# Optimization experiments

Hardware: AMD Instinct MI355X
Metric: run time of the kernel (lower is better)

## Reference

```python
import jax, jax.numpy as jnp
import numpy as np

B, L, C = 2, 2048, 1024
DK, H = 64, 16

def setup_inputs() -> dict:
    key = jax.random.key(0)
    ks = jax.random.split(key, 12)
    def lin(kw, kb, out_dim, in_dim):
        w = jax.random.normal(kw, (out_dim, in_dim), jnp.float32) * (1.0 / np.sqrt(in_dim))
        b = jnp.zeros((out_dim,), jnp.float32)
        return w, b
    WQ_w, WQ_b = lin(ks[0], ks[1], DK * H, C)
    WK_w, WK_b = lin(ks[2], ks[3], DK * H, C)
    WV_w, WV_b = lin(ks[4], ks[5], DK * H, C)
    WO_w, WO_b = lin(ks[6], ks[7], C, DK * H)
    qx = jax.random.normal(ks[8], (B, L, C), jnp.float32)
    kx = jax.random.normal(ks[9], (B, L, C), jnp.float32)
    vx = jax.random.normal(ks[10], (B, L, C), jnp.float32)
    maskPAD = jax.random.randint(ks[11], (B, L, L), 0, 2, jnp.int32)
    return {"qx": qx, "kx": kx, "vx": vx, "maskPAD": maskPAD,
            "WQ_w": WQ_w, "WQ_b": WQ_b, "WK_w": WK_w, "WK_b": WK_b,
            "WV_w": WV_w, "WV_b": WV_b, "WO_w": WO_w, "WO_b": WO_b}

def reference(qx, kx, vx, maskPAD, WQ_w, WQ_b, WK_w, WK_b, WV_w, WV_b, WO_w, WO_b):
    Bq, qL, _ = qx.shape
    kvL = kx.shape[1]
    # projections -> [B, H, L, DK]
    q = (qx @ WQ_w.T + WQ_b).reshape(Bq, qL, H, DK).transpose(0, 2, 1, 3)
    k = (kx @ WK_w.T + WK_b).reshape(Bq, kvL, H, DK).transpose(0, 2, 1, 3)
    v = (vx @ WV_w.T + WV_b).reshape(Bq, kvL, H, DK).transpose(0, 2, 1, 3)
    scores = jnp.einsum('bhqd,bhkd->bhqk', q, k) / np.sqrt(DK).astype(np.float32)
    scores = jnp.where((maskPAD == 0)[:, None, :, :], jnp.float32(-2**15 + 1), scores)
    alpha = jax.nn.softmax(scores, axis=3)  # dropout p=0 (eval)
    z = jnp.einsum('bhqk,bhkd->bhqd', alpha, v)
    z = z.transpose(0, 2, 1, 3).reshape(Bq, qL, H * DK)
    return z @ WO_w.T + WO_b
```

## Files before the change

### kernel.cpp

```cpp
#include <hip/hip_runtime.h>
#include <stdint.h>
#include <math.h>

typedef short short8 __attribute__((ext_vector_type(8)));
typedef short short4v __attribute__((ext_vector_type(4)));
typedef float float4v __attribute__((ext_vector_type(4)));
typedef float float2v __attribute__((ext_vector_type(2)));

static __device__ __forceinline__ float bf2f(uint16_t u) {
    union { uint32_t i; float f; } x; x.i = ((uint32_t)u) << 16; return x.f;
}
static __device__ __forceinline__ uint16_t f2bf(float f) {
    union { float f; uint32_t i; } x; x.f = f;
    uint32_t u = x.i;
    u += 0x7FFFu + ((u >> 16) & 1u);
    return (uint16_t)(u >> 16);
}
static __device__ __forceinline__ uint16_t f2bf_sane(float f) {
    uint16_t u = f2bf(f);
    if ((u & 0x7F80u) == 0x7F80u) u = 0;
    return u;
}
static __device__ __forceinline__ float san_f32(float f) {
    union { float f; uint32_t i; } x; x.f = f;
    if (((x.i >> 23) & 0xFFu) == 0xFFu) return 0.f;
    return x.f;
}
static __device__ __forceinline__ void gll16(const void* g, void* l) {
    __builtin_amdgcn_global_load_lds((const __attribute__((address_space(1))) void*)g,
                                     (__attribute__((address_space(3))) void*)l,
                                     16, 0, 0);
}
static __device__ __forceinline__ short8 load8(const void* p, size_t off, int fp32) {
    if (!fp32) return *(const short8*)((const uint16_t*)p + off);
    const float* f = (const float*)p + off;
    const float4v a = *(const float4v*)f;
    const float4v b = *(const float4v*)(f + 4);
    short8 r;
    r[0] = (short)f2bf(a[0]); r[1] = (short)f2bf(a[1]);
    r[2] = (short)f2bf(a[2]); r[3] = (short)f2bf(a[3]);
    r[4] = (short)f2bf(b[0]); r[5] = (short)f2bf(b[1]);
    r[6] = (short)f2bf(b[2]); r[7] = (short)f2bf(b[3]);
    return r;
}

static __device__ __forceinline__ float fexp2(float x) {
#if __has_builtin(__builtin_amdgcn_exp2f)
    return __builtin_amdgcn_exp2f(x);
#else
    float r; asm("v_exp_f32 %0, %1\ns_nop 0" : "=v"(r) : "v"(x)); return r;
#endif
}

static __device__ __forceinline__ float maskexp2(float s, uint32_t nib, int r) {
    union { float f; uint32_t u; } x; x.f = s;
    const uint32_t keep = (uint32_t)(((int32_t)(nib << (31 - r))) >> 31);
    x.u = (x.u & keep) | (~keep & 0xFF800000u);
    return fexp2(x.f);
}

static __device__ __forceinline__ float4v mfma16_bf16(short4v a, short4v b, float4v c) {
#if __has_builtin(__builtin_amdgcn_mfma_f32_16x16x16bf16_1k)
    return __builtin_amdgcn_mfma_f32_16x16x16bf16_1k(a, b, c, 0, 0, 0);
#else
    float4v d = c;
    asm volatile("v_mfma_f32_16x16x16_bf16 %0, %1, %2, %0"
                 : "+v"(d) : "v"(a), "v"(b));
    return d;
#endif
}

__global__ __launch_bounds__(256) void pack_kernel(
    const int* __restrict__ mask, uint64_t* __restrict__ mask64,
    const uint16_t* __restrict__ qx, int* __restrict__ flag)
{
    const int wave = threadIdx.x >> 6, lane = threadIdx.x & 63;
    if (blockIdx.x == 1024) {
        __shared__ int s;
        const int tid = threadIdx.x;
        if (tid == 0) s = 0;
        __syncthreads();
        int bad = 0;
#pragma unroll 8
        for (int i = 0; i < 64; ++i) {
            const uint16_t u = qx[tid * 64 + i];
            bad |= ((u & 0x7F80u) == 0x7F80u) ? 1 : 0;
        }
        if (bad) atomicOr(&s, 1);
        __syncthreads();
        if (tid == 0) *flag = s;
        return;
    }
    const int row = blockIdx.x * 4 + wave;
    const int* src = mask + (size_t)row * 2048;
#pragma unroll 4
    for (int j = 0; j < 32; ++j) {
        const int m = src[j * 64 + lane];
        const uint64_t bal = __ballot(m != 0);
        if (lane == 0) mask64[(size_t)row * 32 + j] = bal;
    }
}

__global__ __launch_bounds__(256) void convert_kernel(
    const void* qx, const void* kx, const void* vx,
    const void* wq, const void* wk, const void* wv, const void* wo,
    const void* bq, const void* bk, const void* bv, const void* bo,
    uint16_t* cIn, uint16_t* cW, uint16_t* cB, const int* flag)
{
    const int mode = *flag;
    if (!mode) return;
    const int z = blockIdx.z;
    if (z < 3) {
        const void* src = (z == 0) ? qx : (z == 1) ? kx : vx;
        uint16_t* dst = cIn + (size_t)z * 4194304;
#pragma unroll
        for (int it = 0; it < 8; ++it) {
            const int idx8 = (blockIdx.x * 8 + it) * 256 + threadIdx.x;
            *(short8*)(dst + (size_t)idx8 * 8) = load8(src, (size_t)idx8 * 8, 1);
        }
    } else if (z < 7) {
        const int t = z - 3;
        const void* src = (t == 0) ? wq : (t == 1) ? wk : (t == 2) ? wv : wo;
        uint16_t* dst = cW + (size_t)t * 1048576;
#pragma unroll
        for (int it = 0; it < 2; ++it) {
            const int idx8 = (blockIdx.x * 2 + it) * 256 + threadIdx.x;
            *(short8*)(dst + (size_t)idx8 * 8) = load8(src, (size_t)idx8 * 8, 1);
        }
    } else {
        const int idx8 = blockIdx.x * 256 + threadIdx.x;
        if (idx8 < 128) {
#pragma unroll
            for (int t = 0; t < 4; ++t) {
                const void* src = (t == 0) ? bq : (t == 1) ? bk : (t == 2) ? bv : bo;
                *(short8*)(cB + t * 1024 + idx8 * 8) = load8(src, (size_t)idx8 * 8, 1);
            }
        }
    }
}

template <int MI, int NI>
static __device__ __forceinline__ void gemm_tile(
    const uint16_t* __restrict__ A, const uint16_t* __restrict__ W,
    const uint16_t* __restrict__ bias, void* __restrict__ C,
    int c_fp32, float out_scale)
{
    constexpr int TM = MI * 32, TN = NI * 32;
    __shared__ __align__(16) uint16_t sA[TM * 32];
    __shared__ __align__(16) uint16_t sB[TN * 32];

    const int tid  = threadIdx.x;
    const int wave = tid >> 6;
    const int lane = tid & 63;
    const int quad = lane >> 4;
    const int l15  = lane & 15;
    const int m0 = blockIdx.y * TM;
    const int n0 = blockIdx.x * TN;
    const int wm = (wave >> 1) * (MI * 16);
    const int wn = (wave & 1) * (NI * 16);
    const int r16 = lane >> 2;
    const int ch  = lane & 3;

    float4v acc[MI][NI] = {};

    for (int k0 = 0; k0 < 1024; k0 += 32) {
        __syncthreads();
#pragma unroll
        for (int g = wave; g < TM / 16; g += 4)
            gll16(A + (size_t)(m0 + g * 16 + r16) * 1024 + k0 + ch * 8,
                  (char*)sA + (size_t)g * 1024);
#pragma unroll
        for (int g = wave; g < TN / 16; g += 4)
            gll16(W + (size_t)(n0 + g * 16 + r16) * 1024 + k0 + ch * 8,
                  (char*)sB + (size_t)g * 1024);
        asm volatile("s_waitcnt vmcnt(0)" ::: "memory");
        __syncthreads();

        short8 af[MI], bfr[NI];
#pragma unroll
        for (int i = 0; i < MI; ++i)
            af[i] = *(const short8*)&sA[(wm + i * 16 + l15) * 32 + quad * 8];
#pragma unroll
        for (int j = 0; j < NI; ++j)
            bfr[j] = *(const short8*)&sB[(wn + j * 16 + l15) * 32 + quad * 8];
#pragma unroll
        for (int mi = 0; mi < MI; ++mi)
#pragma unroll
            for (int ni = 0; ni < NI; ++ni)
                acc[mi][ni] = __builtin_amdgcn_mfma_f32_16x16x32_bf16(
                    af[mi], bfr[ni], acc[mi][ni], 0, 0, 0);
    }

#pragma unroll
    for (int ni = 0; ni < NI; ++ni) {
        const int n = n0 + wn + ni * 16 + l15;
        const float bv = bf2f(bias[n]);
#pragma unroll
        for (int mi = 0; mi < MI; ++mi) {
            const int mbase = m0 + wm + mi * 16 + quad * 4;
#pragma unroll
            for (int r = 0; r < 4; ++r) {
                const float v = (acc[mi][ni][r] + bv) * out_scale;
                const size_t idx = (size_t)(mbase + r) * 1024 + n;
                if (c_fp32) ((float*)C)[idx] = san_f32(v);
                else        ((uint16_t*)C)[idx] = f2bf_sane(v);
            }
        }
    }
}

__global__ __launch_bounds__(256) void qkv_kernel(
    const uint16_t* rqx, const uint16_t* rkx, const uint16_t* rvx,
    const uint16_t* rwq, const uint16_t* rwk, const uint16_t* rwv,
    const uint16_t* rbq, const uint16_t* rbk, const uint16_t* rbv,
    const uint16_t* cIn, const uint16_t* cW, const uint16_t* cB,
    uint16_t* Q, uint16_t* K, uint16_t* V, const int* flag)
{
    const int mode = *flag;
    const int z = blockIdx.z;
    const uint16_t* A = mode ? cIn + (size_t)z * 4194304
                             : ((z == 0) ? rqx : (z == 1) ? rkx : rvx);
    const uint16_t* W = mode ? cW + (size_t)z * 1048576
                             : ((z == 0) ? rwq : (z == 1) ? rwk : rwv);
    const uint16_t* b = mode ? cB + z * 1024
                             : ((z == 0) ? rbq : (z == 1) ? rbk : rbv);
    uint16_t* C = (z == 0) ? Q : (z == 1) ? K : V;
    const float sc = (z == 0) ? 0.18033688f : 1.0f;
    gemm_tile<4, 4>(A, W, b, C, 0, sc);
}

__global__ __launch_bounds__(256) void out_kernel(
    const uint16_t* Z, const uint16_t* rwo, const uint16_t* rbo,
    const uint16_t* cW, const uint16_t* cB, void* out, const int* flag)
{
    const int mode = *flag;
    const uint16_t* W = mode ? cW + 3 * 1048576 : rwo;
    const uint16_t* b = mode ? cB + 3 * 1024 : rbo;
    gemm_tile<2, 4>(Z, W, b, out, mode, 1.0f);
}

__global__ __launch_bounds__(256) void vtrans_kernel(
    const uint16_t* __restrict__ Vp, uint16_t* __restrict__ Vt)
{
    __shared__ __align__(16) uint16_t t[64][72];
    const int tid = threadIdx.x;
    const int lt = blockIdx.x, h = blockIdx.y, b = blockIdx.z;
#pragma unroll
    for (int p = 0; p < 2; ++p) {
        const int r = p * 32 + (tid >> 3);
        const int c = (tid & 7) * 8;
        *(short8*)&t[r][c] =
            *(const short8*)(Vp + (size_t)(b * 2048 + lt * 64 + r) * 1024 + h * 64 + c);
    }
    __syncthreads();
#pragma unroll
    for (int p = 0; p < 2; ++p) {
        const int d = p * 32 + (tid >> 3);
        const int c = (tid & 7) * 8;
        short8 v;
#pragma unroll
        for (int j = 0; j < 8; ++j) v[j] = (short)t[c + j][d];
        *(short8*)(Vt + (size_t)((b * 16 + h) * 64 + d) * 2048 + lt * 64 + c) = v;
    }
}

#define VS 72

__global__ __launch_bounds__(256, 4) void attn_kernel(
    const uint16_t* __restrict__ Q, const uint16_t* __restrict__ Kp,
    const uint16_t* __restrict__ Vt, const uint64_t* __restrict__ mask64,
    uint16_t* __restrict__ Oa, uint16_t* __restrict__ Ob,
    uint16_t* __restrict__ Oc, float* __restrict__ lpart)
{
    __shared__ __align__(16) uint16_t sK[64 * VS];
    __shared__ __align__(16) uint16_t sV[64 * VS];

    const int tid = threadIdx.x;
    const int wave = tid >> 6, lane = tid & 63;
    const int quad = lane >> 4, l15 = lane & 15;
    const int qt = blockIdx.x, h = blockIdx.y;
    const int b = blockIdx.z & 1, seg = blockIdx.z >> 1;
    const int q0 = qt * 128;
    const int qw = q0 + wave * 32;

    const int srow = tid >> 2;
    const int sc0  = tid & 3;

    short8 qf[2][2];
#pragma unroll
    for (int mi = 0; mi < 2; ++mi)
#pragma unroll
        for (int kk = 0; kk < 2; ++kk)
            qf[mi][kk] = *(const short8*)(Q + (size_t)(b * 2048 + qw + mi * 16 + l15) * 1024
                                            + h * 64 + (quad + 4 * kk) * 8);

    const uint64_t* mrow[2];
#pragma unroll
    for (int mj = 0; mj < 2; ++mj)
        mrow[mj] = mask64 + (size_t)(b * 2048 + qw + mj * 16 + l15) * 32;

    const uint16_t* Kbase = Kp + (size_t)(b * 2048 + srow) * 1024 + h * 64;
    const uint16_t* Vbase = Vt + (size_t)((b * 16 + h) * 64 + srow) * 2048;

    float4v oaccT[4][2] = {};
    float2v lsum2[2] = {};

    const int kt_lo = seg * 11;
    const int kt_hi = (seg == 2) ? 32 : kt_lo + 11;

    short8 kx0 = *(const short8*)(Kbase + (size_t)(kt_lo * 64) * 1024 + sc0 * 8);
    short8 kx1 = *(const short8*)(Kbase + (size_t)(kt_lo * 64) * 1024 + (sc0 + 4) * 8);
    short8 vx0 = *(const short8*)(Vbase + kt_lo * 64 + sc0 * 8);
    short8 vx1 = *(const short8*)(Vbase + kt_lo * 64 + (sc0 + 4) * 8);

    for (int kt = kt_lo; kt < kt_hi; ++kt) {
        const uint64_t mwq0 = mrow[0][kt] >> (quad * 4);
        const uint64_t mwq1 = mrow[1][kt] >> (quad * 4);
        __syncthreads();
        *(short8*)&sK[srow * VS + sc0 * 8]       = kx0;
        *(short8*)&sK[srow * VS + (sc0 + 4) * 8] = kx1;
        *(short8*)&sV[srow * VS + sc0 * 8]       = vx0;
        *(short8*)&sV[srow * VS + (sc0 + 4) * 8] = vx1;
        __syncthreads();

        short8 nk0, nk1, nv0, nv1;
        if (kt + 1 < kt_hi) {
            const int k0n = (kt + 1) * 64;
            nk0 = *(const short8*)(Kbase + (size_t)k0n * 1024 + sc0 * 8);
            nk1 = *(const short8*)(Kbase + (size_t)k0n * 1024 + (sc0 + 4) * 8);
            nv0 = *(const short8*)(Vbase + k0n + sc0 * 8);
            nv1 = *(const short8*)(Vbase + k0n + (sc0 + 4) * 8);
        } else {
            nk0 = kx0; nk1 = kx1; nv0 = vx0; nv1 = vx1;
        }

        float4v sacc[2][4] = {};
        __builtin_amdgcn_s_setprio(1);
#pragma unroll
        for (int ni = 0; ni < 4; ++ni) {
            const int row = ni * 16 + l15;
#pragma unroll
            for (int kk = 0; kk < 2; ++kk) {
                const short8 kf = *(const short8*)&sK[row * VS + (quad + 4 * kk) * 8];
                sacc[0][ni] = __builtin_amdgcn_mfma_f32_16x16x32_bf16(kf, qf[0][kk], sacc[0][ni], 0, 0, 0);
                sacc[1][ni] = __builtin_amdgcn_mfma_f32_16x16x32_bf16(kf, qf[1][kk], sacc[1][ni], 0, 0, 0);
            }
        }
        __builtin_amdgcn_s_setprio(0);

        short4v pf[2][4];
#pragma unroll
        for (int mj = 0; mj < 2; ++mj) {
            const uint64_t mwq = mj ? mwq1 : mwq0;
#pragma unroll
            for (int ni = 0; ni < 4; ++ni) {
                const uint32_t nib = (uint32_t)(mwq >> (ni * 16)) & 0xFu;
                const float p0 = maskexp2(sacc[mj][ni][0], nib, 0);
                const float p1 = maskexp2(sacc[mj][ni][1], nib, 1);
                const float p2 = maskexp2(sacc[mj][ni][2], nib, 2);
                const float p3 = maskexp2(sacc[mj][ni][3], nib, 3);
                float2v lo; lo[0] = p0; lo[1] = p1;
                float2v hi; hi[0] = p2; hi[1] = p3;
                lsum2[mj] += lo;
                lsum2[mj] += hi;
                short4v t;
                t[0] = (short)f2bf(p0);
                t[1] = (short)f2bf(p1);
                t[2] = (short)f2bf(p2);
                t[3] = (short)f2bf(p3);
                pf[mj][ni] = t;
            }
        }

        __builtin_amdgcn_s_setprio(1);
#pragma unroll
        for (int di = 0; di < 4; ++di) {
            const int row = di * 16 + l15;
#pragma unroll
            for (int ni = 0; ni < 4; ++ni) {
                const short4v vf = *(const short4v*)&sV[row * VS + ni * 16 + quad * 4];
                oaccT[di][0] = mfma16_bf16(vf, pf[0][ni], oaccT[di][0]);
                oaccT[di][1] = mfma16_bf16(vf, pf[1][ni], oaccT[di][1]);
            }
        }
        __builtin_amdgcn_s_setprio(0);

        kx0 = nk0; kx1 = nk1; vx0 = nv0; vx1 = nv1;
    }

#if !__has_builtin(__builtin_amdgcn_mfma_f32_16x16x16bf16_1k)
    asm volatile("s_nop 7\ns_nop 7\ns_nop 7" ::: "memory");
#endif

    float lsum[2];
#pragma unroll
    for (int mj = 0; mj < 2; ++mj) lsum[mj] = lsum2[mj][0] + lsum2[mj][1];

#pragma unroll
    for (int mj = 0; mj < 2; ++mj) {
        lsum[mj] += __shfl_xor(lsum[mj], 16);
        lsum[mj] += __shfl_xor(lsum[mj], 32);
    }

    uint16_t* Op = (seg == 0) ? Oa : (seg == 1) ? Ob : Oc;
#pragma unroll
    for (int mj = 0; mj < 2; ++mj) {
        const int qrow = qw + mj * 16 + l15;
#pragma unroll
        for (int di = 0; di < 4; ++di) {
            short4v o;
#pragma unroll
            for (int r = 0; r < 4; ++r) o[r] = (short)f2bf(oaccT[di][mj][r]);
            *(short4v*)(Op + (size_t)(b * 2048 + qrow) * 1024 + h * 64 + di * 16 + quad * 4) = o;
        }
        if (quad == 0)
            lpart[seg * 65536 + (b * 16 + h) * 2048 + qrow] = lsum[mj];
    }
}

__global__ __launch_bounds__(256) void combine_kernel(
    const uint16_t* __restrict__ Oa, const uint16_t* __restrict__ Ob,
    const uint16_t* __restrict__ Oc, const float* __restrict__ lpart,
    uint16_t* __restrict__ Z)
{
    const int e8 = blockIdx.x * 256 + threadIdx.x;
    const int flat = e8 * 8;
    const int bh_row = flat >> 10;
    const int h = (flat >> 6) & 15;
    const int b = bh_row >> 11;
    const int row = bh_row & 2047;
    const int lidx = (b * 16 + h) * 2048 + row;
    const float inv = 1.0f / fmaxf(lpart[lidx] + lpart[65536 + lidx] + lpart[131072 + lidx], 1e-37f);
    const short8 a = *(const short8*)(Oa + flat);
    const short8 c = *(const short8*)(Ob + flat);
    const short8 d = *(const short8*)(Oc + flat);
    short8 o;
#pragma unroll
    for (int j = 0; j < 8; ++j)
        o[j] = (short)f2bf_sane((bf2f((uint16_t)a[j]) + bf2f((uint16_t)c[j]) + bf2f((uint16_t)d[j])) * inv);
    *(short8*)(Z + flat) = o;
}

extern "C" void kernel_launch(void* const* d_in, const int* in_sizes, int n_in,
                              void* d_out, int out_size, void* d_ws, size_t ws_size,
                              hipStream_t stream)
{
    const void* qx  = d_in[0];
    const void* kx  = d_in[1];
    const void* vx  = d_in[2];
    const int*  msk = (const int*)d_in[3];

    char* ws = (char*)d_ws;
    const size_t MB = 1024 * 1024;
    uint16_t* cIn = (uint16_t*)(ws);
    uint16_t* cW  = (uint16_t*)(ws + 24 * MB);
    uint16_t* cB  = (uint16_t*)(ws + 32 * MB);
    int*      flg = (int*)(ws + 32 * MB + 16 * 1024);
    uint16_t* Qb  = (uint16_t*)(ws + 33 * MB);
    uint16_t* Kb  = (uint16_t*)(ws + 41 * MB);
    uint16_t* Vb  = (uint16_t*)(ws + 49 * MB);
    uint64_t* m64 = (uint64_t*)(ws + 57 * MB);
    uint16_t* Vt  = (uint16_t*)(ws + 8 * MB);
    uint16_t* Oa  = (uint16_t*)(ws);
    uint16_t* Ob  = (uint16_t*)(ws + 16 * MB);
    uint16_t* Oc  = (uint16_t*)(ws + 49 * MB);
    float*    lp  = (float*)(ws + 24 * MB);
    uint16_t* Zb  = Oa;

    pack_kernel<<<1025, 256, 0, stream>>>(msk, m64, (const uint16_t*)qx, flg);
    convert_kernel<<<dim3(256, 1, 8), 256, 0, stream>>>(
        qx, kx, vx, d_in[4], d_in[6], d_in[8], d_in[10],
        d_in[5], d_in[7], d_in[9], d_in[11], cIn, cW, cB, flg);
    qkv_kernel<<<dim3(8, 32, 3), 256, 0, stream>>>(
        (const uint16_t*)qx, (const uint16_t*)kx, (const uint16_t*)vx,
        (const uint16_t*)d_in[4], (const uint16_t*)d_in[6], (const uint16_t*)d_in[8],
        (const uint16_t*)d_in[5], (const uint16_t*)d_in[7], (const uint16_t*)d_in[9],
        cIn, cW, cB, Qb, Kb, Vb, flg);
    vtrans_kernel<<<dim3(32, 16, 2), 256, 0, stream>>>(Vb, Vt);
    attn_kernel<<<dim3(16, 16, 6), 256, 0, stream>>>(Qb, Kb, Vt, m64, Oa, Ob, Oc, lp);
    combine_kernel<<<4096, 256, 0, stream>>>(Oa, Ob, Oc, lp, Zb);
    out_kernel<<<dim3(8, 64), 256, 0, stream>>>(
        Zb, (const uint16_t*)d_in[10], (const uint16_t*)d_in[11], cW, cB, d_out, flg);
}
```

Baseline: 300.1 us.

## Fuse V transpose into QKV GEMM epilogue and use hardware bf16 conversion

The V projection GEMM now writes its output directly in the transposed [B,H,DK,L] layout, which removes the separate vtrans kernel launch and its extra round trip through global memory. The workspace layout is shuffled so that Vt and Oc no longer alias. The attention kernel also switches its P and O float-to-bf16 conversions to the hip_bf16 intrinsic, which may lower to hardware conversion instructions. The transposed store writes 4-element column chunks with a 2048-element stride, so it is less coalesced than the row-major store it replaces.

Result: no change. 301.1 us (+0.3%).

```diff
diff --git a/kernel.cpp b/kernel.cpp
--- a/kernel.cpp
+++ b/kernel.cpp
@@ -1,4 +1,5 @@
 #include <hip/hip_runtime.h>
+#include <hip/hip_bf16.h>
 #include <stdint.h>
 #include <math.h>
 
@@ -15,6 +16,10 @@
     uint32_t u = x.i;
     u += 0x7FFFu + ((u >> 16) & 1u);
     return (uint16_t)(u >> 16);
+}
+static __device__ __forceinline__ uint16_t f2bf_hw(float f) {
+    __hip_bfloat16 h = __float2bfloat16(f);
+    uint16_t u; __builtin_memcpy(&u, &h, 2); return u;
 }
 static __device__ __forceinline__ uint16_t f2bf_sane(float f) {
     uint16_t u = f2bf(f);
@@ -143,7 +148,7 @@
 static __device__ __forceinline__ void gemm_tile(
     const uint16_t* __restrict__ A, const uint16_t* __restrict__ W,
     const uint16_t* __restrict__ bias, void* __restrict__ C,
-    int c_fp32, float out_scale)
+    int c_fp32, float out_scale, int vt)
 {
     constexpr int TM = MI * 32, TN = NI * 32;
     __shared__ __align__(16) uint16_t sA[TM * 32];
@@ -191,6 +196,26 @@
                     af[mi], bfr[ni], acc[mi][ni], 0, 0, 0);
     }
 
+    if (vt) {
+#pragma unroll
+        for (int ni = 0; ni < NI; ++ni) {
+            const int n = n0 + wn + ni * 16 + l15;
+            const float bv = bf2f(bias[n]);
+            const int hh = n >> 6, dd = n & 63;
+#pragma unroll
+            for (int mi = 0; mi < MI; ++mi) {
+                const int mbase = m0 + wm + mi * 16 + quad * 4;
+                const int bb = mbase >> 11, l0 = mbase & 2047;
+                short4v o;
+#pragma unroll
+                for (int r = 0; r < 4; ++r)
+                    o[r] = (short)f2bf_sane(acc[mi][ni][r] + bv);
+                *(short4v*)((uint16_t*)C + ((size_t)((bb * 16 + hh) * 64 + dd)) * 2048 + l0) = o;
+            }
+        }
+        return;
+    }
+
 #pragma unroll
     for (int ni = 0; ni < NI; ++ni) {
         const int n = n0 + wn + ni * 16 + l15;
@@ -214,7 +239,7 @@
     const uint16_t* rwq, const uint16_t* rwk, const uint16_t* rwv,
     const uint16_t* rbq, const uint16_t* rbk, const uint16_t* rbv,
     const uint16_t* cIn, const uint16_t* cW, const uint16_t* cB,
-    uint16_t* Q, uint16_t* K, uint16_t* V, const int* flag)
+    uint16_t* Q, uint16_t* K, uint16_t* Vt, const int* flag)
 {
     const int mode = *flag;
     const int z = blockIdx.z;
@@ -224,9 +249,9 @@
                              : ((z == 0) ? rwq : (z == 1) ? rwk : rwv);
     const uint16_t* b = mode ? cB + z * 1024
                              : ((z == 0) ? rbq : (z == 1) ? rbk : rbv);
-    uint16_t* C = (z == 0) ? Q : (z == 1) ? K : V;
+    uint16_t* C = (z == 0) ? Q : (z == 1) ? K : Vt;
     const float sc = (z == 0) ? 0.18033688f : 1.0f;
-    gemm_tile<4, 4>(A, W, b, C, 0, sc);
+    gemm_tile<4, 4>(A, W, b, C, 0, sc, z == 2);
 }
 
 __global__ __launch_bounds__(256) void out_kernel(
@@ -236,32 +261,7 @@
     const int mode = *flag;
     const uint16_t* W = mode ? cW + 3 * 1048576 : rwo;
     const uint16_t* b = mode ? cB + 3 * 1024 : rbo;
-    gemm_tile<2, 4>(Z, W, b, out, mode, 1.0f);
-}
-
-__global__ __launch_bounds__(256) void vtrans_kernel(
-    const uint16_t* __restrict__ Vp, uint16_t* __restrict__ Vt)
-{
-    __shared__ __align__(16) uint16_t t[64][72];
-    const int tid = threadIdx.x;
-    const int lt = blockIdx.x, h = blockIdx.y, b = blockIdx.z;
-#pragma unroll
-    for (int p = 0; p < 2; ++p) {
-        const int r = p * 32 + (tid >> 3);
-        const int c = (tid & 7) * 8;
-        *(short8*)&t[r][c] =
-            *(const short8*)(Vp + (size_t)(b * 2048 + lt * 64 + r) * 1024 + h * 64 + c);
-    }
-    __syncthreads();
-#pragma unroll
-    for (int p = 0; p < 2; ++p) {
-        const int d = p * 32 + (tid >> 3);
-        const int c = (tid & 7) * 8;
-        short8 v;
-#pragma unroll
-        for (int j = 0; j < 8; ++j) v[j] = (short)t[c + j][d];
-        *(short8*)(Vt + (size_t)((b * 16 + h) * 64 + d) * 2048 + lt * 64 + c) = v;
-    }
+    gemm_tile<2, 4>(Z, W, b, out, mode, 1.0f, 0);
 }
 
 #define VS 72
@@ -364,10 +364,10 @@
                 lsum2[mj] += lo;
                 lsum2[mj] += hi;
                 short4v t;
-                t[0] = (short)f2bf(p0);
-                t[1] = (short)f2bf(p1);
-                t[2] = (short)f2bf(p2);
-                t[3] = (short)f2bf(p3);
+                t[0] = (short)f2bf_hw(p0);
+                t[1] = (short)f2bf_hw(p1);
+                t[2] = (short)f2bf_hw(p2);
+                t[3] = (short)f2bf_hw(p3);
                 pf[mj][ni] = t;
             }
         }
@@ -410,7 +410,7 @@
         for (int di = 0; di < 4; ++di) {
             short4v o;
 #pragma unroll
-            for (int r = 0; r < 4; ++r) o[r] = (short)f2bf(oaccT[di][mj][r]);
+            for (int r = 0; r < 4; ++r) o[r] = (short)f2bf_hw(oaccT[di][mj][r]);
             *(short4v*)(Op + (size_t)(b * 2048 + qrow) * 1024 + h * 64 + di * 16 + quad * 4) = o;
         }
         if (quad == 0)
@@ -458,12 +458,11 @@
     int*      flg = (int*)(ws + 32 * MB + 16 * 1024);
     uint16_t* Qb  = (uint16_t*)(ws + 33 * MB);
     uint16_t* Kb  = (uint16_t*)(ws + 41 * MB);
-    uint16_t* Vb  = (uint16_t*)(ws + 49 * MB);
+    uint16_t* Vt  = (uint16_t*)(ws + 49 * MB);
     uint64_t* m64 = (uint64_t*)(ws + 57 * MB);
-    uint16_t* Vt  = (uint16_t*)(ws + 8 * MB);
     uint16_t* Oa  = (uint16_t*)(ws);
+    uint16_t* Oc  = (uint16_t*)(ws + 8 * MB);
     uint16_t* Ob  = (uint16_t*)(ws + 16 * MB);
-    uint16_t* Oc  = (uint16_t*)(ws + 49 * MB);
     float*    lp  = (float*)(ws + 24 * MB);
     uint16_t* Zb  = Oa;
 
@@ -475,8 +474,7 @@
         (const uint16_t*)qx, (const uint16_t*)kx, (const uint16_t*)vx,
         (const uint16_t*)d_in[4], (const uint16_t*)d_in[6], (const uint16_t*)d_in[8],
         (const uint16_t*)d_in[5], (const uint16_t*)d_in[7], (const uint16_t*)d_in[9],
-        cIn, cW, cB, Qb, Kb, Vb, flg);
-    vtrans_kernel<<<dim3(32, 16, 2), 256, 0, stream>>>(Vb, Vt);
+        cIn, cW, cB, Qb, Kb, Vt, flg);
     attn_kernel<<<dim3(16, 16, 6), 256, 0, stream>>>(Qb, Kb, Vt, m64, Oa, Ob, Oc, lp);
     combine_kernel<<<4096, 256, 0, stream>>>(Oa, Ob, Oc, lp, Zb);
     out_kernel<<<dim3(8, 64), 256, 0, stream>>>(
```

## Remap GEMM workgroups per XCD for L2 locality and use hardware bf16 convert

Applied to the files above, without the earlier changes.

Remaps the workgroup IDs in the QKV and output projection GEMMs so that each XCD (blocks are dispatched round-robin by wgid mod 8) processes a contiguous band of M-panels, which is meant to improve L2 reuse of the A and W tiles. It also swaps the software round-to-nearest float-to-bf16 conversion in the attention P-matrix and output stores for the HIP intrinsic, which may lower to a hardware convert instruction on gfx950. The remap hardcodes grid dimensions (8 x 32 x 3 and 8 x 64), so it depends on the launch shape. The intrinsic's rounding and NaN behavior may differ slightly from the manual routine.

Measured after the change: 294.8 us. Within noise of the previous version (-1.8%).

```diff
diff --git a/kernel.cpp b/kernel.cpp
--- a/kernel.cpp
+++ b/kernel.cpp
@@ -1,4 +1,5 @@
 #include <hip/hip_runtime.h>
+#include <hip/hip_bf16.h>
 #include <stdint.h>
 #include <math.h>
 
@@ -15,6 +16,10 @@
     uint32_t u = x.i;
     u += 0x7FFFu + ((u >> 16) & 1u);
     return (uint16_t)(u >> 16);
+}
+static __device__ __forceinline__ uint16_t f2bf_hw(float f) {
+    __hip_bfloat16 h = __float2bfloat16(f);
+    uint16_t u; __builtin_memcpy(&u, &h, 2); return u;
 }
 static __device__ __forceinline__ uint16_t f2bf_sane(float f) {
     uint16_t u = f2bf(f);
@@ -143,7 +148,7 @@
 static __device__ __forceinline__ void gemm_tile(
     const uint16_t* __restrict__ A, const uint16_t* __restrict__ W,
     const uint16_t* __restrict__ bias, void* __restrict__ C,
-    int c_fp32, float out_scale)
+    int c_fp32, float out_scale, int bx, int by)
 {
     constexpr int TM = MI * 32, TN = NI * 32;
     __shared__ __align__(16) uint16_t sA[TM * 32];
@@ -154,8 +159,8 @@
     const int lane = tid & 63;
     const int quad = lane >> 4;
     const int l15  = lane & 15;
-    const int m0 = blockIdx.y * TM;
-    const int n0 = blockIdx.x * TN;
+    const int m0 = by * TM;
+    const int n0 = bx * TN;
     const int wm = (wave >> 1) * (MI * 16);
     const int wn = (wave & 1) * (NI * 16);
     const int r16 = lane >> 2;
@@ -217,7 +222,14 @@
     uint16_t* Q, uint16_t* K, uint16_t* V, const int* flag)
 {
     const int mode = *flag;
-    const int z = blockIdx.z;
+    const int wgid = blockIdx.x + (blockIdx.y << 3) + (blockIdx.z << 8);
+    const int xcd = wgid & 7;
+    const int s   = wgid >> 3;
+    const int panel = xcd * 12 + (s >> 3);
+    const int bx = s & 7;
+    const int z  = panel >> 5;
+    const int by = panel & 31;
+
     const uint16_t* A = mode ? cIn + (size_t)z * 4194304
                              : ((z == 0) ? rqx : (z == 1) ? rkx : rvx);
     const uint16_t* W = mode ? cW + (size_t)z * 1048576
@@ -226,7 +238,7 @@
                              : ((z == 0) ? rbq : (z == 1) ? rbk : rbv);
     uint16_t* C = (z == 0) ? Q : (z == 1) ? K : V;
     const float sc = (z == 0) ? 0.18033688f : 1.0f;
-    gemm_tile<4, 4>(A, W, b, C, 0, sc);
+    gemm_tile<4, 4>(A, W, b, C, 0, sc, bx, by);
 }
 
 __global__ __launch_bounds__(256) void out_kernel(
@@ -236,7 +248,12 @@
     const int mode = *flag;
     const uint16_t* W = mode ? cW + 3 * 1048576 : rwo;
     const uint16_t* b = mode ? cB + 3 * 1024 : rbo;
-    gemm_tile<2, 4>(Z, W, b, out, mode, 1.0f);
+    const int wgid = blockIdx.x + (blockIdx.y << 3);
+    const int xcd = wgid & 7;
+    const int s   = wgid >> 3;
+    const int by  = xcd * 8 + (s >> 3);
+    const int bx  = s & 7;
+    gemm_tile<2, 4>(Z, W, b, out, mode, 1.0f, bx, by);
 }
 
 __global__ __launch_bounds__(256) void vtrans_kernel(
@@ -364,10 +381,10 @@
                 lsum2[mj] += lo;
                 lsum2[mj] += hi;
                 short4v t;
-                t[0] = (short)f2bf(p0);
-                t[1] = (short)f2bf(p1);
-                t[2] = (short)f2bf(p2);
-                t[3] = (short)f2bf(p3);
+                t[0] = (short)f2bf_hw(p0);
+                t[1] = (short)f2bf_hw(p1);
+                t[2] = (short)f2bf_hw(p2);
+                t[3] = (short)f2bf_hw(p3);
                 pf[mj][ni] = t;
             }
         }
@@ -410,7 +427,7 @@
         for (int di = 0; di < 4; ++di) {
             short4v o;
 #pragma unroll
-            for (int r = 0; r < 4; ++r) o[r] = (short)f2bf(oaccT[di][mj][r]);
+            for (int r = 0; r < 4; ++r) o[r] = (short)f2bf_hw(oaccT[di][mj][r]);
             *(short4v*)(Op + (size_t)(b * 2048 + qrow) * 1024 + h * 64 + di * 16 + quad * 4) = o;
         }
         if (quad == 0)
```
